# Optimization experiments

Hardware: AMD Instinct MI355X
Metric: run time of the kernel (lower is better)

## Reference

```python
import jax, jax.numpy as jnp
import numpy as np

DIM = 256
NUM_HEADS = 4
HEAD_DIM = DIM // NUM_HEADS


def setup_inputs() -> dict:
    key = jax.random.key(0)
    ks = jax.random.split(key, 8)
    B, N, C = 4, 2048, DIM
    x = jax.random.normal(ks[0], (B, N, C), dtype=jnp.float32)
    R = jax.random.normal(ks[1], (B, 3, 3), dtype=jnp.float32)
    P = jax.random.normal(ks[2], (N, 3), dtype=jnp.float32)
    s = 1.0 / np.sqrt(C)
    qkv_w = jax.random.normal(ks[3], (3 * C, C), dtype=jnp.float32) * s
    qkv_b = jax.random.normal(ks[4], (3 * C,), dtype=jnp.float32) * 0.02
    proj_w = jax.random.normal(ks[5], (C, C), dtype=jnp.float32) * s
    proj_b = jax.random.normal(ks[6], (C,), dtype=jnp.float32) * 0.02
    pos_scale = jnp.asarray(1.0, dtype=jnp.float32)
    return {"x": x, "R": R, "P": P, "qkv_w": qkv_w, "qkv_b": qkv_b,
            "proj_w": proj_w, "proj_b": proj_b, "pos_scale": pos_scale}


def reference(x, R, P, qkv_w, qkv_b, proj_w, proj_b, pos_scale):
    B, N, C = x.shape
    H, D = NUM_HEADS, HEAD_DIM
    scale = D ** -0.5
    # qkv: (B,N,3C) -> (3,B,H,N,D)
    qkv = (x @ qkv_w.T + qkv_b).reshape(B, N, 3, H, D).transpose(2, 0, 3, 1, 4)
    q, k, v = qkv[0], qkv[1], qkv[2]
    # attention logits (B,H,N,N)
    attn = jnp.einsum('bhid,bhjd->bhij', q, k) * scale
    # positional bias: RP = (R @ P^T)^T -> (B,N,3); bias_ij = dot(RP_i, P_j)
    RP = jnp.einsum('bab,jb->bja', R, P) if False else jnp.einsum('bca,ja->bjc', jnp.swapaxes(R, 1, 2), P)
    RP = jnp.einsum('bcd,jd->bjc', R, P)  # (B,N,3): (R @ P.T).T
    bias = jnp.einsum('bik,jk->bij', RP, P)[:, None, :, :] * pos_scale  # (B,1,N,N) broadcast over heads
    attn = jax.nn.softmax(attn + bias, axis=-1)
    out = jnp.einsum('bhij,bhjd->bhid', attn, v)  # (B,H,N,D)
    out = out.transpose(0, 2, 1, 3).reshape(B, N, C)
    out = out @ proj_w.T + proj_b
    return out
```

## Files before the change

### kernel.cpp

```cpp
#include <hip/hip_runtime.h>
#include <hip/hip_bf16.h>

#define B_ 4
#define N_ 2048
#define C_ 256
#define H_ 4
#define D_ 64

typedef __attribute__((ext_vector_type(8))) short bf16x8;
typedef __attribute__((ext_vector_type(4))) float f32x4;

#define LOG2E 1.4426950408889634f

static __device__ inline unsigned short f2bf(float f) {
    unsigned u = __builtin_bit_cast(unsigned, f);
    unsigned r = (u + 0x7fffu + ((u >> 16) & 1u)) >> 16;
    return (unsigned short)r;
}
static __device__ inline float bf2f(unsigned short h) {
    unsigned u = ((unsigned)h) << 16;
    return __builtin_bit_cast(float, u);
}
static __device__ inline unsigned pack2(float a, float b) {
    __hip_bfloat162 h = __float22bfloat162_rn(make_float2(a, b));
    unsigned u;
    __builtin_memcpy(&u, &h, 4);
    return u;
}
static __device__ inline bf16x8 ld_frag(const unsigned short* p) {
    return __builtin_bit_cast(bf16x8, *(const uint4*)p);
}
static __device__ inline void gload_lds16(const unsigned short* g, unsigned short* l) {
    __builtin_amdgcn_global_load_lds(
        (const __attribute__((address_space(1))) unsigned int*)(g),
        (__attribute__((address_space(3))) unsigned int*)(l),
        16, 0, 0);
}
template<int CTRL>
static __device__ inline float fmax_dpp(float x) {
    int yi = __builtin_amdgcn_update_dpp(0, __builtin_bit_cast(int, x),
                                         CTRL, 0xf, 0xf, true);
    return fmaxf(x, __builtin_bit_cast(float, yi));
}

__global__ __launch_bounds__(256) void cvt_kernel(
    const float* __restrict__ x, const float* __restrict__ qkv_w,
    const float* __restrict__ proj_w, const float* __restrict__ Pm,
    unsigned short* __restrict__ xb, unsigned short* __restrict__ wqb,
    unsigned short* __restrict__ wpb, unsigned short* __restrict__ eb)
{
    const int bid = blockIdx.x, tid = threadIdx.x;
    if (bid >= 1152) {
        const int n = (bid - 1152) * 256 + tid;
        const float* pp = Pm + n * 3;
        float p0 = pp[0], p1 = pp[1], p2 = pp[2];
        unsigned u0 = f2bf(p0), u1 = f2bf(p1), u2 = f2bf(p2);
        unsigned v0 = f2bf(p0 - bf2f((unsigned short)u0));
        unsigned v1 = f2bf(p1 - bf2f((unsigned short)u1));
        unsigned v2 = f2bf(p2 - bf2f((unsigned short)u2));
        uint4 lo, hi;
        lo.x = u0 | (u1 << 16); lo.y = u2 | (v0 << 16);
        lo.z = v1 | (v2 << 16); lo.w = u0 | (u1 << 16);
        hi.x = u2; hi.y = 0u; hi.z = 0u; hi.w = 0u;
        *(uint4*)&eb[n * 16 + 0] = lo;
        *(uint4*)&eb[n * 16 + 8] = hi;
        return;
    }
    const float* s; unsigned short* d; int i;
    if (bid < 1024)      { s = x;      d = xb;  i = (bid * 256 + tid) * 8; }
    else if (bid < 1120) { s = qkv_w;  d = wqb; i = ((bid - 1024) * 256 + tid) * 8; }
    else                 { s = proj_w; d = wpb; i = ((bid - 1120) * 256 + tid) * 8; }
    float4 a = *(const float4*)(s + i);
    float4 b = *(const float4*)(s + i + 4);
    uint4 u;
    u.x = pack2(a.x, a.y); u.y = pack2(a.z, a.w);
    u.z = pack2(b.x, b.y); u.w = pack2(b.z, b.w);
    *(uint4*)(d + i) = u;
}

__global__ __launch_bounds__(256) void qkv_gemm(
    const unsigned short* __restrict__ xb, const unsigned short* __restrict__ wb,
    const float* __restrict__ bias, unsigned short* __restrict__ qb,
    unsigned short* __restrict__ kb, unsigned short* __restrict__ vt)
{
    __shared__ __align__(16) unsigned short As[2][128 * 64];
    __shared__ __align__(16) unsigned short Bs[2][128 * 64];
    const int m0 = blockIdx.x * 128, o0 = blockIdx.y * 128;
    const int tid = threadIdx.x;
    const int wave = tid >> 6, lane = tid & 63, quad = lane >> 4, l16 = lane & 15;
    const int wy = wave >> 1, wx = wave & 1;
    const int x7 = l16 & 7;
    const int rl = lane >> 3, sl = lane & 7;
    const int swz = (sl ^ rl) * 8;

    const unsigned short* aq0 = &xb[(size_t)(m0 + 32 * wave + rl) * 256 + swz];
    const unsigned short* bq0 = &wb[(size_t)(o0 + 32 * wave + rl) * 256 + swz];

    auto ISSUE = [&](int buf, int k0) {
        unsigned short* ad = &As[buf][(32 * wave) * 64];
        unsigned short* bd = &Bs[buf][(32 * wave) * 64];
        #pragma unroll
        for (int i = 0; i < 4; ++i) {
            gload_lds16(aq0 + (size_t)(8 * i) * 256 + k0, ad + (8 * i) * 64);
            gload_lds16(bq0 + (size_t)(8 * i) * 256 + k0, bd + (8 * i) * 64);
        }
    };

    f32x4 acc[4][4];
    #pragma unroll
    for (int i = 0; i < 4; ++i)
        #pragma unroll
        for (int j = 0; j < 4; ++j) acc[i][j] = (f32x4){0.f, 0.f, 0.f, 0.f};

    ISSUE(0, 0);

    #pragma unroll
    for (int t = 0; t < 4; ++t) {
        const int cur = t & 1;
        asm volatile("s_waitcnt vmcnt(0)" ::: "memory");
        __builtin_amdgcn_s_barrier();
        __builtin_amdgcn_sched_barrier(0);
        if (t < 3) ISSUE(cur ^ 1, (t + 1) * 64);
        __builtin_amdgcn_s_setprio(1);
        #pragma unroll
        for (int ks = 0; ks < 2; ++ks) {
            bf16x8 a[4], b[4];
            #pragma unroll
            for (int mt = 0; mt < 4; ++mt)
                a[mt] = ld_frag(&As[cur][(wy * 64 + mt * 16 + l16) * 64
                                         + (((ks * 4 + quad) ^ x7) * 8)]);
            #pragma unroll
            for (int nt = 0; nt < 4; ++nt)
                b[nt] = ld_frag(&Bs[cur][(wx * 64 + nt * 16 + l16) * 64
                                         + (((ks * 4 + quad) ^ x7) * 8)]);
            #pragma unroll
            for (int mt = 0; mt < 4; ++mt)
                #pragma unroll
                for (int nt = 0; nt < 4; ++nt)
                    acc[mt][nt] = __builtin_amdgcn_mfma_f32_16x16x32_bf16(a[mt], b[nt], acc[mt][nt], 0, 0, 0);
        }
        __builtin_amdgcn_s_setprio(0);
    }

    const int sec = o0 + wx * 64;
    const int three = sec >> 8;
    const int h = (sec >> 6) & 3;
    const int b = m0 >> 11;
    float bv[4];
    #pragma unroll
    for (int nt = 0; nt < 4; ++nt) bv[nt] = bias[sec + nt * 16 + l16];

    if (three == 2) {
        const int n64 = (m0 + wy * 64) & 2047;
        const size_t bh64 = ((size_t)b * H_ + h) * 64;
        #pragma unroll
        for (int nt = 0; nt < 4; ++nt) {
            int d = nt * 16 + l16;
            #pragma unroll
            for (int r = 0; r < 4; ++r) {
                ushort4 v;
                v.x = f2bf(acc[0][nt][r] + bv[nt]);
                v.y = f2bf(acc[1][nt][r] + bv[nt]);
                v.z = f2bf(acc[2][nt][r] + bv[nt]);
                v.w = f2bf(acc[3][nt][r] + bv[nt]);
                *(ushort4*)&vt[(bh64 + d) * N_ + n64 + 16 * quad + 4 * r] = v;
            }
        }
    } else {
        unsigned short* dst = (three == 0) ? qb : kb;
        float sc = (three == 0) ? (0.125f * LOG2E) : 1.0f;
        #pragma unroll
        for (int mt = 0; mt < 4; ++mt)
            #pragma unroll
            for (int r = 0; r < 4; ++r) {
                int n = (m0 + wy * 64 + mt * 16 + quad * 4 + r) & 2047;
                size_t rowbase = (((size_t)b * H_ + h) * N_ + n) * D_;
                #pragma unroll
                for (int nt = 0; nt < 4; ++nt)
                    dst[rowbase + nt * 16 + l16] = f2bf((acc[mt][nt][r] + bv[nt]) * sc);
            }
    }
}

#define LDK 64

__global__ __launch_bounds__(256) void attn_kernel(
    const unsigned short* __restrict__ qb, const unsigned short* __restrict__ kb,
    const unsigned short* __restrict__ vt, const unsigned short* __restrict__ eb,
    const float* __restrict__ Rm, const float* __restrict__ Pm,
    const float* __restrict__ ps_ptr,
    unsigned short* __restrict__ Opart, float* __restrict__ ml)
{
    __shared__ __align__(16) unsigned short Ks[2][64 * LDK];
    __shared__ __align__(16) unsigned short Vs[2][64 * LDK];
    __shared__ __align__(16) unsigned short Ps[64 * LDK];

    const int bh = blockIdx.y;
    const int b = bh >> 2;
    const int i0 = blockIdx.x * 64;
    const int split = blockIdx.z;
    const int tid = threadIdx.x;
    const int wave = tid >> 6, lane = tid & 63;
    const int quad = lane >> 4, l16 = lane & 15;
    const int x7 = l16 & 7;
    const float ps = ps_ptr[0];

    const size_t base = (size_t)bh * N_ * D_;
    const unsigned short* qg = qb + base;
    const unsigned short* kg = kb + base;
    const unsigned short* vg = vt + base;

    const int jbeg = split * (N_ / 4);

    const int rl = lane >> 3, sl = lane & 7;
    const int swz = (sl ^ rl) * 8;
    const unsigned short* kq = kg + (size_t)(jbeg + wave * 16 + rl) * D_ + swz;
    const unsigned short* vq = vg + (size_t)(wave * 16 + rl) * N_ + jbeg + swz;
    const unsigned short* ep = eb + (size_t)(jbeg + l16) * 16 + (quad & 1) * 8;

    auto ISSUE_K = [&](int nb) {
        unsigned short* kd = &Ks[nb][(wave * 16) * LDK];
        gload_lds16(kq,          kd);
        gload_lds16(kq + 8 * D_, kd + 8 * LDK);
        kq += 64 * D_;
    };
    auto ISSUE_V = [&](int nb) {
        unsigned short* vd = &Vs[nb][(wave * 16) * LDK];
        gload_lds16(vq,          vd);
        gload_lds16(vq + 8 * N_, vd + 8 * LDK);
        vq += 64;
    };
    auto LOAD_E = [&](bf16x8 (&e)[4]) {
        #pragma unroll
        for (int t = 0; t < 4; ++t) e[t] = ld_frag(ep + t * 256);
        ep += 64 * 16;
    };

    ISSUE_K(0);
    bf16x8 eA[4], eB[4];
    LOAD_E(eA);

    const int qrow = i0 + wave * 16 + l16;
    bf16x8 aq[3];
    #pragma unroll
    for (int ks = 0; ks < 2; ++ks)
        aq[ks] = ld_frag(&qg[(size_t)qrow * D_ + ks * 32 + quad * 8]);

    {
        float p0 = Pm[qrow * 3 + 0], p1 = Pm[qrow * 3 + 1], p2 = Pm[qrow * 3 + 2];
        float sc = ps * LOG2E;
        unsigned short ah[3], al[3];
        #pragma unroll
        for (int c = 0; c < 3; ++c) {
            float a = (Rm[b * 9 + c * 3 + 0] * p0 + Rm[b * 9 + c * 3 + 1] * p1
                     + Rm[b * 9 + c * 3 + 2] * p2) * sc;
            ah[c] = f2bf(a);
            al[c] = f2bf(a - bf2f(ah[c]));
        }
        bf16x8 e = (bf16x8){0,0,0,0,0,0,0,0};
        if (quad == 0) {
            e[0] = (short)ah[0]; e[1] = (short)ah[1]; e[2] = (short)ah[2];
            e[3] = (short)ah[0]; e[4] = (short)ah[1]; e[5] = (short)ah[2];
            e[6] = (short)al[0]; e[7] = (short)al[1];
        } else if (quad == 1) {
            e[0] = (short)al[2];
        }
        aq[2] = e;
    }

    const bf16x8 ones = (bf16x8){0x3F80,0x3F80,0x3F80,0x3F80,0x3F80,0x3F80,0x3F80,0x3F80};

    float m_run = -1e30f;
    f32x4 o_acc[4], lacc;
    #pragma unroll
    for (int t = 0; t < 4; ++t) o_acc[t] = (f32x4){0.f, 0.f, 0.f, 0.f};
    lacc = (f32x4){0.f, 0.f, 0.f, 0.f};

    f32x4 sA[4], sB[4];

    auto S_COMPUTE = [&](f32x4 (&sc)[4], int kb_, bf16x8 (&ec)[4]) {
        __builtin_amdgcn_s_setprio(1);
        #pragma unroll
        for (int t = 0; t < 4; ++t) {
            const int rb = (l16 + 16 * t) * LDK;
            f32x4 c = {0.f, 0.f, 0.f, 0.f};
            #pragma unroll
            for (int ks = 0; ks < 2; ++ks) {
                bf16x8 bk = ld_frag(&Ks[kb_][rb + (((ks * 4 + quad) ^ x7) * 8)]);
                c = __builtin_amdgcn_mfma_f32_16x16x32_bf16(aq[ks], bk, c, 0, 0, 0);
            }
            c = __builtin_amdgcn_mfma_f32_16x16x32_bf16(aq[2], ec[t], c, 0, 0, 0);
            sc[t] = c;
        }
        __builtin_amdgcn_s_setprio(0);
    };

    auto SOFTMAX = [&](f32x4 (&s)[4]) {
        float mt[4];
        #pragma unroll
        for (int t = 0; t < 4; ++t)
            mt[t] = fmaxf(fmaxf(s[t][0], s[t][1]), fmaxf(s[t][2], s[t][3]));
        float mx = fmaxf(fmaxf(mt[0], mt[1]), fmaxf(mt[2], mt[3]));
        mx = fmax_dpp<0xB1>(mx);
        mx = fmax_dpp<0x4E>(mx);
        mx = fmax_dpp<0x124>(mx);
        mx = fmax_dpp<0x128>(mx);
        if (__any(mx > m_run + 8.0f)) {
            float mnew = fmaxf(m_run, mx);
            float alpha = exp2f(m_run - mnew);
            #pragma unroll
            for (int t = 0; t < 4; ++t)
                #pragma unroll
                for (int r = 0; r < 4; ++r)
                    o_acc[t][r] *= alpha;
            #pragma unroll
            for (int r = 0; r < 4; ++r) lacc[r] *= alpha;
            m_run = mnew;
        }
        #pragma unroll
        for (int r = 0; r < 4; ++r) {
            float p0 = exp2f(s[0][r] - m_run), p1 = exp2f(s[1][r] - m_run);
            float p2 = exp2f(s[2][r] - m_run), p3 = exp2f(s[3][r] - m_run);
            uint2 w;
            w.x = pack2(p0, p1);
            w.y = pack2(p2, p3);
            const int prow = quad * 4 + r;
            *(uint2*)&Ps[(wave * 16 + prow) * LDK
                         + (((l16 >> 1) ^ (prow & 7)) * 8) + (l16 & 1) * 4] = w;
        }
    };

    auto PV = [&](int vb_) {
        __builtin_amdgcn_s_setprio(1);
        #pragma unroll
        for (int ks = 0; ks < 2; ++ks) {
            bf16x8 ap = ld_frag(&Ps[(wave * 16 + l16) * LDK
                                    + (((ks * 4 + quad) ^ x7) * 8)]);
            #pragma unroll
            for (int t = 0; t < 4; ++t) {
                bf16x8 bv = ld_frag(&Vs[vb_][(l16 + 16 * t) * LDK
                                             + (((ks * 4 + quad) ^ x7) * 8)]);
                o_acc[t] = __builtin_amdgcn_mfma_f32_16x16x32_bf16(ap, bv, o_acc[t], 0, 0, 0);
            }
            lacc = __builtin_amdgcn_mfma_f32_16x16x32_bf16(ap, ones, lacc, 0, 0, 0);
        }
        __builtin_amdgcn_s_setprio(0);
    };

    auto STEP = [&](int cur, bool more, f32x4 (&snew)[4], f32x4 (&sold)[4],
                    bf16x8 (&euse)[4], bf16x8 (&eload)[4]) {
        asm volatile("s_waitcnt vmcnt(0)" ::: "memory");
        __builtin_amdgcn_s_barrier();
        __builtin_amdgcn_sched_barrier(0);
        if (more) ISSUE_K(cur ^ 1);
        ISSUE_V(cur);
        SOFTMAX(sold);
        S_COMPUTE(snew, cur, euse);
        if (more) LOAD_E(eload);
        PV(cur ^ 1);
    };

    asm volatile("s_waitcnt vmcnt(0)" ::: "memory");
    __builtin_amdgcn_s_barrier();
    __builtin_amdgcn_sched_barrier(0);
    ISSUE_K(1);
    ISSUE_V(0);
    S_COMPUTE(sA, 0, eA);
    LOAD_E(eB);

    #pragma unroll 1
    for (int it = 0; it < 3; ++it) {
        STEP(1, true, sB, sA, eB, eA);
        STEP(0, true, sA, sB, eA, eB);
    }
    STEP(1, false, sB, sA, eB, eA);

    asm volatile("s_waitcnt vmcnt(0)" ::: "memory");
    __builtin_amdgcn_s_barrier();
    __builtin_amdgcn_sched_barrier(0);
    SOFTMAX(sB);
    PV(1);

    const size_t pbase = (size_t)(split * 16 + bh) * N_;
    #pragma unroll
    for (int r = 0; r < 4; ++r) {
        int row = i0 + wave * 16 + quad * 4 + r;
        #pragma unroll
        for (int t = 0; t < 4; ++t)
            Opart[(pbase + row) * D_ + l16 + 16 * t] = f2bf(o_acc[t][r]);
        if (l16 == 0) {
            float2* mlp = (float2*)ml;
            mlp[pbase + row] = make_float2(m_run, lacc[r]);
        }
    }
}

__global__ __launch_bounds__(256) void proj_gemm(
    const unsigned short* __restrict__ Opart, const float* __restrict__ ml,
    const unsigned short* __restrict__ wb, const float* __restrict__ bias,
    float* __restrict__ out)
{
    __shared__ __align__(16) unsigned short As[2][64 * 64];
    __shared__ __align__(16) unsigned short Bs[2][64 * 64];
    const int m0 = blockIdx.x * 64, o0 = blockIdx.y * 64;
    const int tid = threadIdx.x;
    const int wave = tid >> 6, lane = tid & 63, quad = lane >> 4, l16 = lane & 15;
    const int x7 = l16 & 7;
    const int rl = lane >> 3, sl = lane & 7;
    const int swz = (sl ^ rl) * 8;
    const float2* mlp = (const float2*)ml;

    const int srow = tid >> 2, sc16 = (tid & 3) * 16;
    const int s0 = (tid & 3) * 2;
    const int sm = m0 + srow, sb = sm >> 11, sn = sm & 2047;

    float wgt[4][4];
    #pragma unroll
    for (int h = 0; h < 4; ++h) {
        size_t r1 = (size_t)(sb * 4 + h) * N_ + sn;
        float2 m0v = mlp[r1], m1v = mlp[r1 + 16 * N_];
        float2 m2v = mlp[r1 + 32 * N_], m3v = mlp[r1 + 48 * N_];
        float mm = fmaxf(fmaxf(m0v.x, m1v.x), fmaxf(m2v.x, m3v.x));
        float w0 = exp2f(m0v.x - mm), w1 = exp2f(m1v.x - mm);
        float w2 = exp2f(m2v.x - mm), w3 = exp2f(m3v.x - mm);
        float inv = 1.f / (m0v.y * w0 + m1v.y * w1 + m2v.y * w2 + m3v.y * w3);
        wgt[h][0] = w0 * inv; wgt[h][1] = w1 * inv;
        wgt[h][2] = w2 * inv; wgt[h][3] = w3 * inv;
    }

    const unsigned short* bq0 = &wb[(size_t)(o0 + 16 * wave + rl) * 256 + swz];
    auto ISSUE_B = [&](int buf, int k0) {
        unsigned short* bd = &Bs[buf][(16 * wave) * 64];
        gload_lds16(bq0 + k0,           bd);
        gload_lds16(bq0 + 8 * 256 + k0, bd + 8 * 64);
    };

    union U16 { uint4 u; unsigned short s[8]; };
    U16 ar[4][2];
    auto LOAD_A = [&](int h) {
        size_t r1 = (size_t)(sb * 4 + h) * N_ + sn;
        #pragma unroll
        for (int s = 0; s < 4; ++s) {
            const unsigned short* p = &Opart[(r1 + (size_t)(16 * s) * N_) * D_ + sc16];
            ar[s][0].u = *(const uint4*)(p);
            ar[s][1].u = *(const uint4*)(p + 8);
        }
    };

    ISSUE_B(0, 0);
    LOAD_A(0);

    f32x4 acc[4];
    #pragma unroll
    for (int j = 0; j < 4; ++j) acc[j] = (f32x4){0.f, 0.f, 0.f, 0.f};

    #pragma unroll
    for (int t = 0; t < 4; ++t) {
        const int cur = t & 1;
        {
            float w0 = wgt[t][0], w1 = wgt[t][1], w2 = wgt[t][2], w3 = wgt[t][3];
            #pragma unroll
            for (int j = 0; j < 2; ++j) {
                uint4 mv;
                unsigned* mp = (unsigned*)&mv;
                #pragma unroll
                for (int q = 0; q < 4; ++q) {
                    float lo = bf2f(ar[0][j].s[2*q])   * w0 + bf2f(ar[1][j].s[2*q])   * w1
                             + bf2f(ar[2][j].s[2*q])   * w2 + bf2f(ar[3][j].s[2*q])   * w3;
                    float hi = bf2f(ar[0][j].s[2*q+1]) * w0 + bf2f(ar[1][j].s[2*q+1]) * w1
                             + bf2f(ar[2][j].s[2*q+1]) * w2 + bf2f(ar[3][j].s[2*q+1]) * w3;
                    mp[q] = pack2(lo, hi);
                }
                *(uint4*)&As[cur][srow * 64 + (((s0 + j) ^ (srow & 7)) * 8)] = mv;
            }
        }
        __syncthreads();
        if (t < 3) {
            ISSUE_B(cur ^ 1, (t + 1) * 64);
            LOAD_A(t + 1);
        }
        __builtin_amdgcn_s_setprio(1);
        #pragma unroll
        for (int ks = 0; ks < 2; ++ks) {
            bf16x8 a = ld_frag(&As[cur][(wave * 16 + l16) * 64
                                        + (((ks * 4 + quad) ^ x7) * 8)]);
            #pragma unroll
            for (int nt = 0; nt < 4; ++nt) {
                bf16x8 b = ld_frag(&Bs[cur][(nt * 16 + l16) * 64
                                            + (((ks * 4 + quad) ^ x7) * 8)]);
                acc[nt] = __builtin_amdgcn_mfma_f32_16x16x32_bf16(a, b, acc[nt], 0, 0, 0);
            }
        }
        __builtin_amdgcn_s_setprio(0);
    }

    float bv[4];
    #pragma unroll
    for (int nt = 0; nt < 4; ++nt) bv[nt] = bias[o0 + nt * 16 + l16];
    #pragma unroll
    for (int r = 0; r < 4; ++r) {
        int m = m0 + wave * 16 + quad * 4 + r;
        #pragma unroll
        for (int nt = 0; nt < 4; ++nt)
            out[(size_t)m * 256 + o0 + nt * 16 + l16] = acc[nt][r] + bv[nt];
    }
}

extern "C" void kernel_launch(void* const* d_in, const int* in_sizes, int n_in,
                              void* d_out, int out_size, void* d_ws, size_t ws_size,
                              hipStream_t stream) {
    const float* x       = (const float*)d_in[0];
    const float* Rm      = (const float*)d_in[1];
    const float* Pm      = (const float*)d_in[2];
    const float* qkv_w   = (const float*)d_in[3];
    const float* qkv_b   = (const float*)d_in[4];
    const float* proj_w  = (const float*)d_in[5];
    const float* proj_b  = (const float*)d_in[6];
    const float* pos_scl = (const float*)d_in[7];
    float* out = (float*)d_out;

    const size_t NE = (size_t)B_ * H_ * N_ * D_;
    unsigned short* opart = (unsigned short*)d_ws;
    unsigned short* qb    = opart + 4 * NE;
    unsigned short* kb    = qb   + NE;
    unsigned short* vtb   = kb   + NE;
    float*          mlb   = (float*)(vtb + NE);
    unsigned short* eb    = (unsigned short*)(mlb + (size_t)4 * 16 * N_ * 2);
    unsigned short* wqb   = eb  + 2048 * 16;
    unsigned short* wpb   = wqb + 768 * 256;
    unsigned short* xb    = opart;

    cvt_kernel<<<1160, 256, 0, stream>>>(x, qkv_w, proj_w, Pm, xb, wqb, wpb, eb);
    qkv_gemm<<<dim3(64, 6), 256, 0, stream>>>(xb, wqb, qkv_b, qb, kb, vtb);
    attn_kernel<<<dim3(32, 16, 4), 256, 0, stream>>>(qb, kb, vtb, eb, Rm, Pm, pos_scl, opart, mlb);
    proj_gemm<<<dim3(128, 4), 256, 0, stream>>>(opart, mlb, wpb, proj_b, out);
}
```

Measured before the change: 134.3 us.

## Use 8-wave 128-row attention blocks sharing K/V tiles with single-buffered V

```diff
diff --git a/kernel.cpp b/kernel.cpp
--- a/kernel.cpp
+++ b/kernel.cpp
@@ -184,7 +184,7 @@
 
 #define LDK 64
 
-__global__ __launch_bounds__(256) void attn_kernel(
+__global__ __launch_bounds__(512, 8) void attn_kernel(
     const unsigned short* __restrict__ qb, const unsigned short* __restrict__ kb,
     const unsigned short* __restrict__ vt, const unsigned short* __restrict__ eb,
     const float* __restrict__ Rm, const float* __restrict__ Pm,
@@ -192,12 +192,12 @@
     unsigned short* __restrict__ Opart, float* __restrict__ ml)
 {
     __shared__ __align__(16) unsigned short Ks[2][64 * LDK];
-    __shared__ __align__(16) unsigned short Vs[2][64 * LDK];
-    __shared__ __align__(16) unsigned short Ps[64 * LDK];
+    __shared__ __align__(16) unsigned short Vs[64 * LDK];
+    __shared__ __align__(16) unsigned short Ps[128 * LDK];
 
     const int bh = blockIdx.y;
     const int b = bh >> 2;
-    const int i0 = blockIdx.x * 64;
+    const int i0 = blockIdx.x * 128;
     const int split = blockIdx.z;
     const int tid = threadIdx.x;
     const int wave = tid >> 6, lane = tid & 63;
@@ -214,20 +214,16 @@
 
     const int rl = lane >> 3, sl = lane & 7;
     const int swz = (sl ^ rl) * 8;
-    const unsigned short* kq = kg + (size_t)(jbeg + wave * 16 + rl) * D_ + swz;
-    const unsigned short* vq = vg + (size_t)(wave * 16 + rl) * N_ + jbeg + swz;
+    const unsigned short* kq = kg + (size_t)(jbeg + wave * 8 + rl) * D_ + swz;
+    const unsigned short* vq = vg + (size_t)(wave * 8 + rl) * N_ + jbeg + swz;
     const unsigned short* ep = eb + (size_t)(jbeg + l16) * 16 + (quad & 1) * 8;
 
     auto ISSUE_K = [&](int nb) {
-        unsigned short* kd = &Ks[nb][(wave * 16) * LDK];
-        gload_lds16(kq,          kd);
-        gload_lds16(kq + 8 * D_, kd + 8 * LDK);
+        gload_lds16(kq, &Ks[nb][(wave * 8) * LDK]);
         kq += 64 * D_;
     };
-    auto ISSUE_V = [&](int nb) {
-        unsigned short* vd = &Vs[nb][(wave * 16) * LDK];
-        gload_lds16(vq,          vd);
-        gload_lds16(vq + 8 * N_, vd + 8 * LDK);
+    auto ISSUE_V = [&]() {
+        gload_lds16(vq, &Vs[(wave * 8) * LDK]);
         vq += 64;
     };
     auto LOAD_E = [&](bf16x8 (&e)[4]) {
@@ -299,8 +295,8 @@
         float mt[4];
         #pragma unroll
         for (int t = 0; t < 4; ++t)
-            mt[t] = fmaxf(fmaxf(s[t][0], s[t][1]), fmaxf(s[t][2], s[t][3]));
-        float mx = fmaxf(fmaxf(mt[0], mt[1]), fmaxf(mt[2], mt[3]));
+            mt[t] = fmaxf(fmaxf(fmaxf(s[t][0], s[t][1]), s[t][2]), s[t][3]);
+        float mx = fmaxf(fmaxf(fmaxf(mt[0], mt[1]), mt[2]), mt[3]);
         mx = fmax_dpp<0xB1>(mx);
         mx = fmax_dpp<0x4E>(mx);
         mx = fmax_dpp<0x124>(mx);
@@ -330,7 +326,7 @@
         }
     };
 
-    auto PV = [&](int vb_) {
+    auto PV = [&]() {
         __builtin_amdgcn_s_setprio(1);
         #pragma unroll
         for (int ks = 0; ks < 2; ++ks) {
@@ -338,8 +334,8 @@
                                     + (((ks * 4 + quad) ^ x7) * 8)]);
             #pragma unroll
             for (int t = 0; t < 4; ++t) {
-                bf16x8 bv = ld_frag(&Vs[vb_][(l16 + 16 * t) * LDK
-                                             + (((ks * 4 + quad) ^ x7) * 8)]);
+                bf16x8 bv = ld_frag(&Vs[(l16 + 16 * t) * LDK
+                                        + (((ks * 4 + quad) ^ x7) * 8)]);
                 o_acc[t] = __builtin_amdgcn_mfma_f32_16x16x32_bf16(ap, bv, o_acc[t], 0, 0, 0);
             }
             lacc = __builtin_amdgcn_mfma_f32_16x16x32_bf16(ap, ones, lacc, 0, 0, 0);
@@ -352,21 +348,26 @@
         asm volatile("s_waitcnt vmcnt(0)" ::: "memory");
         __builtin_amdgcn_s_barrier();
         __builtin_amdgcn_sched_barrier(0);
+        if (more) LOAD_E(eload);
+        ISSUE_V();
         if (more) ISSUE_K(cur ^ 1);
-        ISSUE_V(cur);
+        __builtin_amdgcn_sched_barrier(0);
         SOFTMAX(sold);
         S_COMPUTE(snew, cur, euse);
-        if (more) LOAD_E(eload);
-        PV(cur ^ 1);
+        __builtin_amdgcn_sched_barrier(0);
+        if (more) asm volatile("s_waitcnt vmcnt(1)" ::: "memory");
+        else      asm volatile("s_waitcnt vmcnt(0)" ::: "memory");
+        __builtin_amdgcn_s_barrier();
+        __builtin_amdgcn_sched_barrier(0);
+        PV();
     };
 
     asm volatile("s_waitcnt vmcnt(0)" ::: "memory");
     __builtin_amdgcn_s_barrier();
     __builtin_amdgcn_sched_barrier(0);
     ISSUE_K(1);
-    ISSUE_V(0);
+    LOAD_E(eB);
     S_COMPUTE(sA, 0, eA);
-    LOAD_E(eB);
 
     #pragma unroll 1
     for (int it = 0; it < 3; ++it) {
@@ -378,8 +379,12 @@
     asm volatile("s_waitcnt vmcnt(0)" ::: "memory");
     __builtin_amdgcn_s_barrier();
     __builtin_amdgcn_sched_barrier(0);
+    ISSUE_V();
     SOFTMAX(sB);
-    PV(1);
+    asm volatile("s_waitcnt vmcnt(0)" ::: "memory");
+    __builtin_amdgcn_s_barrier();
+    __builtin_amdgcn_sched_barrier(0);
+    PV();
 
     const size_t pbase = (size_t)(split * 16 + bh) * N_;
     #pragma unroll
@@ -532,6 +537,6 @@
 
     cvt_kernel<<<1160, 256, 0, stream>>>(x, qkv_w, proj_w, Pm, xb, wqb, wpb, eb);
     qkv_gemm<<<dim3(64, 6), 256, 0, stream>>>(xb, wqb, qkv_b, qb, kb, vtb);
-    attn_kernel<<<dim3(32, 16, 4), 256, 0, stream>>>(qb, kb, vtb, eb, Rm, Pm, pos_scl, opart, mlb);
+    attn_kernel<<<dim3(16, 16, 4), 512, 0, stream>>>(qb, kb, vtb, eb, Rm, Pm, pos_scl, opart, mlb);
     proj_gemm<<<dim3(128, 4), 256, 0, stream>>>(opart, mlb, wpb, proj_b, out);
 }
```

Measured after the change: 278.5 us. 107% more time.
